# Performance work log

Hardware: AMD Instinct MI355X
Metric: run time of the kernel (lower is better)

The kernel has to match this reference:

```python
import jax, jax.numpy as jnp
import numpy as np

B = 65536
D_MODEL = 2048
N_EXPERTS = 64
TOP_K = 8
AUX_COEF = 0.01


def setup_inputs() -> dict:
    key = jax.random.key(0)
    kx, kw = jax.random.split(key)
    x = jax.random.normal(kx, (B, D_MODEL), dtype=jnp.float32)
    # nn.Linear(d_model, n_experts, bias=False); stored here as (d_model, n_experts)
    W = jax.random.normal(kw, (D_MODEL, N_EXPERTS), dtype=jnp.float32) / np.sqrt(D_MODEL).astype(np.float32)
    expert_bias = jnp.zeros((N_EXPERTS,), dtype=jnp.float32)
    return {"x": x, "W": W, "expert_bias": expert_bias}


def reference(x, W, expert_bias):
    # router logits: (B, n_experts)
    logits = x @ W
    # topk on bias-shifted logits (aux-loss-free balancing bias)
    biased = logits + expert_bias
    _, indices = jax.lax.top_k(biased, TOP_K)              # (B, top_k) int32
    # softmax over the UNbiased logits of the selected experts
    selected = jnp.take_along_axis(logits, indices, axis=-1)  # (B, top_k)
    gates_topk = jax.nn.softmax(selected, axis=-1)
    # scatter gate weights into sparse (B, n_experts) tensor
    rows = jnp.arange(logits.shape[0])[:, None]
    gates = jnp.zeros_like(logits).at[rows, indices].set(gates_topk)
    # aux load-balance loss (training mode): fraction routed * mean prob
    f_i = (gates > 0).astype(logits.dtype).mean(axis=0)       # (n_experts,)
    P_i = jax.nn.softmax(logits, axis=-1).mean(axis=0)        # (n_experts,)
    aux_loss = AUX_COEF * N_EXPERTS * jnp.sum(f_i * P_i)
    return gates, indices, aux_loss
```

## Files before the change

### kernel.cpp

```cpp
#include <hip/hip_runtime.h>
#include <cstdint>
#include <cstddef>

typedef __attribute__((ext_vector_type(8))) short short8;
typedef __attribute__((ext_vector_type(4))) float f32x4;

#define B_ROWS 65536
#define DMODEL 2048
#define NEXP 64
#define TOPK 8
#define THREADS 256
#define ROWS_PER_BLK 64
#define NBLK (B_ROWS / ROWS_PER_BLK)
#define NKS (DMODEL / 32)
#define SLAB 67
#define GOFF ((size_t)B_ROWS * NEXP)
#define AUX_OFF (GOFF + (size_t)B_ROWS * TOPK)
#define WS_FRAG_OFF 131072

#define GLOAD16(g, l)                                                      \
  __builtin_amdgcn_global_load_lds(                                       \
      (const __attribute__((address_space(1))) void*)(g),                 \
      (__attribute__((address_space(3))) void*)(l), 16, 0, 0)

__device__ __forceinline__ unsigned short bf16_rne(float v, float* back) {
  unsigned u = __float_as_uint(v);
  unsigned r = (u + 0x7FFFu + ((u >> 16) & 1u)) >> 16;
  *back = __uint_as_float(r << 16);
  return (unsigned short)r;
}

__global__ __launch_bounds__(256) void router_prep(
    const float* __restrict__ W, unsigned short* __restrict__ frag)
{
  const int ks = blockIdx.x;
  const int nt = threadIdx.x >> 6;
  const int lane = threadIdx.x & 63;
  const int krow = ks * 32 + (lane >> 4) * 8;
  const int col = nt * 16 + (lane & 15);
  short8 hv, mv, lv;
#pragma unroll
  for (int j = 0; j < 8; ++j) {
    float v = W[(size_t)(krow + j) * NEXP + col];
    float fh, fm, fl;
    unsigned short h = bf16_rne(v, &fh);
    float r = v - fh;
    unsigned short m = bf16_rne(r, &fm);
    float r2 = r - fm;
    unsigned short l = bf16_rne(r2, &fl);
    hv[j] = (short)h; mv[j] = (short)m; lv[j] = (short)l;
  }
  size_t base = (size_t)(ks * 4 + nt) * 1536 + lane * 8;
  *(short8*)(frag + base)        = hv;
  *(short8*)(frag + base + 512)  = mv;
  *(short8*)(frag + base + 1024) = lv;
}

__device__ __forceinline__ void cvt3(float4 a, float4 b,
                                     short8* H, short8* M, short8* L) {
  float f[8] = {a.x, a.y, a.z, a.w, b.x, b.y, b.z, b.w};
#pragma unroll
  for (int j = 0; j < 8; ++j) {
    float fh, fm, fl;
    unsigned short h = bf16_rne(f[j], &fh);
    float r = f[j] - fh;
    unsigned short m = bf16_rne(r, &fm);
    float r2 = r - fm;
    unsigned short l = bf16_rne(r2, &fl);
    (*H)[j] = (short)h; (*M)[j] = (short)m; (*L)[j] = (short)l;
  }
}

#define MFMA __builtin_amdgcn_mfma_f32_16x16x32_bf16

__global__ __launch_bounds__(THREADS, 4) void router_main(
    const float* __restrict__ x, const float* __restrict__ bias,
    const unsigned short* __restrict__ frag, float* __restrict__ out,
    float* __restrict__ ws)
{
  __shared__ __align__(16) float lds[6144];

  const int tid = threadIdx.x;
  const int lane = tid & 63;
  const int w = tid >> 6;
  const size_t row0 = (size_t)blockIdx.x * ROWS_PER_BLK;

  f32x4 acc[4];
#pragma unroll
  for (int nt = 0; nt < 4; ++nt) acc[nt] = (f32x4){0.f, 0.f, 0.f, 0.f};

  const float* xp = x + (row0 + (size_t)w * 16 + (lane & 15)) * DMODEL
                  + (lane >> 4) * 8;

#define STAGE(KS, BUF)                                                     \
  do {                                                                     \
    _Pragma("unroll") for (int j = 0; j < 3; ++j)                          \
      GLOAD16(frag + (size_t)(KS) * 6144 + (w * 3 + j) * 512 + lane * 8,   \
              lds + (BUF) * 3072 + (w * 3 + j) * 256);                     \
  } while (0)

  STAGE(0, 0);
  float4 c0 = *(const float4*)(xp);
  float4 c1 = *(const float4*)(xp + 4);

  for (int ks = 0; ks < NKS; ++ks) {
    __syncthreads();
    float4 n0, n1;
    if (ks + 1 < NKS) {
      STAGE(ks + 1, (ks + 1) & 1);
      n0 = *(const float4*)(xp + (ks + 1) * 32);
      n1 = *(const float4*)(xp + (ks + 1) * 32 + 4);
    }
    const float* bb = lds + (ks & 1) * 3072;
    short8 B[12];
#pragma unroll
    for (int f = 0; f < 12; ++f)
      B[f] = *(const short8*)(bb + f * 256 + lane * 4);
    short8 Ah, Am, Al;
    cvt3(c0, c1, &Ah, &Am, &Al);
#pragma unroll
    for (int nt = 0; nt < 4; ++nt) {
      acc[nt] = MFMA(Ah, B[nt * 3 + 0], acc[nt], 0, 0, 0);
      acc[nt] = MFMA(Ah, B[nt * 3 + 1], acc[nt], 0, 0, 0);
      acc[nt] = MFMA(Am, B[nt * 3 + 0], acc[nt], 0, 0, 0);
      acc[nt] = MFMA(Am, B[nt * 3 + 1], acc[nt], 0, 0, 0);
      acc[nt] = MFMA(Ah, B[nt * 3 + 2], acc[nt], 0, 0, 0);
      acc[nt] = MFMA(Al, B[nt * 3 + 0], acc[nt], 0, 0, 0);
    }
    if (ks + 1 < NKS) { c0 = n0; c1 = n1; }
  }

  __syncthreads();
  float* slab = lds;
#pragma unroll
  for (int nt = 0; nt < 4; ++nt)
#pragma unroll
    for (int reg = 0; reg < 4; ++reg) {
      int row = w * 16 + (lane >> 4) * 4 + reg;
      int col = nt * 16 + (lane & 15);
      slab[row * SLAB + col] = acc[nt][reg];
    }
  __syncthreads();

  if (w == 0) {
    float a[NEXP];
#pragma unroll
    for (int n = 0; n < NEXP; ++n) a[n] = slab[lane * SLAB + n];

    unsigned long long sel = 0ull;
    int idx[TOPK];
    float selu[TOPK];
#pragma unroll
    for (int k = 0; k < TOPK; ++k) {
      float best = -INFINITY, bestu = 0.f;
      int bi = 0;
#pragma unroll
      for (int n = 0; n < NEXP; ++n) {
        float vb = a[n] + bias[n];
        bool taken = (sel >> n) & 1ull;
        vb = taken ? -INFINITY : vb;
        if (vb > best) { best = vb; bestu = a[n]; bi = n; }
      }
      sel |= 1ull << bi;
      idx[k] = bi;
      selu[k] = bestu;
    }

    float mx = selu[0];
#pragma unroll
    for (int k = 1; k < TOPK; ++k) mx = fmaxf(mx, selu[k]);
    float g[TOPK]; float gs = 0.f;
#pragma unroll
    for (int k = 0; k < TOPK; ++k) { g[k] = __expf(selu[k] - mx); gs += g[k]; }
    float ginv = 1.f / gs;

    float* grow = out + (row0 + lane) * NEXP;
#pragma unroll
    for (int n4 = 0; n4 < 16; ++n4) {
      float gv[4];
#pragma unroll
      for (int j = 0; j < 4; ++j) {
        int n = n4 * 4 + j;
        float v = 0.f;
#pragma unroll
        for (int k = 0; k < TOPK; ++k) v = (idx[k] == n) ? g[k] * ginv : v;
        gv[j] = v;
      }
      *(float4*)(grow + n4 * 4) = make_float4(gv[0], gv[1], gv[2], gv[3]);
    }

    float* irow = out + GOFF + (row0 + lane) * TOPK;
    *(float4*)(irow + 0) = make_float4((float)idx[0], (float)idx[1], (float)idx[2], (float)idx[3]);
    *(float4*)(irow + 4) = make_float4((float)idx[4], (float)idx[5], (float)idx[6], (float)idx[7]);

    float m2 = -INFINITY;
#pragma unroll
    for (int n = 0; n < NEXP; ++n) m2 = fmaxf(m2, a[n]);
    float s2 = 0.f;
#pragma unroll
    for (int n = 0; n < NEXP; ++n) s2 += __expf(a[n] - m2);
    float pinv = 1.f / s2;

    float myP = 0.f, myF = 0.f;
#pragma unroll
    for (int n = 0; n < NEXP; ++n) {
      float v = __expf(a[n] - m2) * pinv;
      v += __shfl_xor(v, 1);
      v += __shfl_xor(v, 2);
      v += __shfl_xor(v, 4);
      v += __shfl_xor(v, 8);
      v += __shfl_xor(v, 16);
      v += __shfl_xor(v, 32);
      unsigned long long b = __ballot((sel >> n) & 1ull);
      if (lane == n) { myP = v; myF = (float)__popcll(b); }
    }
    ws[(size_t)blockIdx.x * (2 * NEXP) + lane] = myF;
    ws[(size_t)blockIdx.x * (2 * NEXP) + NEXP + lane] = myP;
  }
}

__global__ __launch_bounds__(256) void router_aux(
    const float* __restrict__ ws, float* __restrict__ out)
{
  __shared__ float sf[4][NEXP];
  __shared__ float sp[4][NEXP];
  int t = threadIdx.x;
  int n = t & 63, part = t >> 6;
  float f = 0.f, p = 0.f;
#pragma unroll 8
  for (int b = part; b < NBLK; b += 4) {
    f += ws[(size_t)b * (2 * NEXP) + n];
    p += ws[(size_t)b * (2 * NEXP) + NEXP + n];
  }
  sf[part][n] = f;
  sp[part][n] = p;
  __syncthreads();
  if (t < NEXP) {
    float F = sf[0][t] + sf[1][t] + sf[2][t] + sf[3][t];
    float P = sp[0][t] + sp[1][t] + sp[2][t] + sp[3][t];
    float v = F * P;
    v += __shfl_xor(v, 1);
    v += __shfl_xor(v, 2);
    v += __shfl_xor(v, 4);
    v += __shfl_xor(v, 8);
    v += __shfl_xor(v, 16);
    v += __shfl_xor(v, 32);
    if (t == 0)
      out[AUX_OFF] = 0.01f * 64.f * v / (4294967296.0f );
  }
}

extern "C" void kernel_launch(void* const* d_in, const int* in_sizes, int n_in,
                              void* d_out, int out_size, void* d_ws, size_t ws_size,
                              hipStream_t stream) {
  const float* x = (const float*)d_in[0];
  const float* W = (const float*)d_in[1];
  const float* bias = (const float*)d_in[2];
  float* out = (float*)d_out;
  float* ws = (float*)d_ws;
  unsigned short* frag = (unsigned short*)(ws + WS_FRAG_OFF);
  router_prep<<<NKS, 256, 0, stream>>>(W, frag);
  router_main<<<NBLK, THREADS, 0, stream>>>(x, bias, frag, out, ws);
  router_aux<<<1, 256, 0, stream>>>(ws, out);
}
```

Before: 216.2 us.

## Stage x tiles into LDS via async global_load_lds and split aux reduction

The main kernel now loads x in 128-column chunks (four k-steps) straight into LDS using async global-to-LDS loads instead of per-thread float4 register loads. The goal is fewer, larger memory transactions that overlap with the MFMA work. This raises LDS use, so occupancy hints drop from 4 to 2 blocks per CU, and there is a manual vmcnt wait. The single-block aux reduction is also split into a 16-block partial pass and a final 64-thread pass, which adds a kernel launch.

```diff
diff --git a/kernel.cpp b/kernel.cpp
--- a/kernel.cpp
+++ b/kernel.cpp
@@ -17,6 +17,10 @@
 #define GOFF ((size_t)B_ROWS * NEXP)
 #define AUX_OFF (GOFF + (size_t)B_ROWS * TOPK)
 #define WS_FRAG_OFF 131072
+#define WS2_OFF 229376
+#define XW 2080
+#define BBASE 8320
+#define LDSF 14464
 
 #define GLOAD16(g, l)                                                      \
   __builtin_amdgcn_global_load_lds(                                       \
@@ -73,12 +77,12 @@
 
 #define MFMA __builtin_amdgcn_mfma_f32_16x16x32_bf16
 
-__global__ __launch_bounds__(THREADS, 4) void router_main(
+__global__ __launch_bounds__(THREADS, 2) void router_main(
     const float* __restrict__ x, const float* __restrict__ bias,
     const unsigned short* __restrict__ frag, float* __restrict__ out,
     float* __restrict__ ws)
 {
-  __shared__ __align__(16) float lds[6144];
+  __shared__ __align__(16) float lds[LDSF];
 
   const int tid = threadIdx.x;
   const int lane = tid & 63;
@@ -89,33 +93,47 @@
 #pragma unroll
   for (int nt = 0; nt < 4; ++nt) acc[nt] = (f32x4){0.f, 0.f, 0.f, 0.f};
 
-  const float* xp = x + (row0 + (size_t)w * 16 + (lane & 15)) * DMODEL
-                  + (lane >> 4) * 8;
-
-#define STAGE(KS, BUF)                                                     \
+  const float* xg = x + (row0 + (size_t)w * 16 + (lane >> 5)) * DMODEL
+                  + (lane & 31) * 4;
+  const int xr_off = w * XW + ((lane & 15) >> 1) * 260 + ((lane & 15) & 1) * 128
+                   + (lane >> 4) * 8;
+
+#define STAGE_X(SC)                                                        \
+  do {                                                                     \
+    _Pragma("unroll") for (int i = 0; i < 8; ++i)                          \
+      GLOAD16(xg + (size_t)i * 2 * DMODEL + (SC) * 128,                    \
+              lds + w * XW + i * 260);                                     \
+  } while (0)
+
+#define STAGE_B(KS, BUF)                                                   \
   do {                                                                     \
     _Pragma("unroll") for (int j = 0; j < 3; ++j)                          \
       GLOAD16(frag + (size_t)(KS) * 6144 + (w * 3 + j) * 512 + lane * 8,   \
-              lds + (BUF) * 3072 + (w * 3 + j) * 256);                     \
+              lds + BBASE + (BUF) * 3072 + (w * 3 + j) * 256);             \
   } while (0)
 
-  STAGE(0, 0);
-  float4 c0 = *(const float4*)(xp);
-  float4 c1 = *(const float4*)(xp + 4);
+  STAGE_X(0);
+  STAGE_B(0, 0);
 
   for (int ks = 0; ks < NKS; ++ks) {
     __syncthreads();
-    float4 n0, n1;
-    if (ks + 1 < NKS) {
-      STAGE(ks + 1, (ks + 1) & 1);
-      n0 = *(const float4*)(xp + (ks + 1) * 32);
-      n1 = *(const float4*)(xp + (ks + 1) * 32 + 4);
-    }
-    const float* bb = lds + (ks & 1) * 3072;
+    if ((ks & 3) == 0 && ks > 0) {
+      STAGE_X(ks >> 2);
+      if (ks + 1 < NKS) STAGE_B(ks + 1, (ks + 1) & 1);
+      asm volatile("s_waitcnt vmcnt(3)" ::: "memory");
+      __builtin_amdgcn_sched_barrier(0);
+    } else {
+      if (ks + 1 < NKS) STAGE_B(ks + 1, (ks + 1) & 1);
+    }
+
+    const float* bb = lds + BBASE + (ks & 1) * 3072;
     short8 B[12];
 #pragma unroll
     for (int f = 0; f < 12; ++f)
       B[f] = *(const short8*)(bb + f * 256 + lane * 4);
+
+    float4 c0 = *(const float4*)(lds + xr_off + (ks & 3) * 32);
+    float4 c1 = *(const float4*)(lds + xr_off + (ks & 3) * 32 + 4);
     short8 Ah, Am, Al;
     cvt3(c0, c1, &Ah, &Am, &Al);
 #pragma unroll
@@ -127,7 +145,6 @@
       acc[nt] = MFMA(Ah, B[nt * 3 + 2], acc[nt], 0, 0, 0);
       acc[nt] = MFMA(Al, B[nt * 3 + 0], acc[nt], 0, 0, 0);
     }
-    if (ks + 1 < NKS) { c0 = n0; c1 = n1; }
   }
 
   __syncthreads();
@@ -219,16 +236,17 @@
   }
 }
 
-__global__ __launch_bounds__(256) void router_aux(
-    const float* __restrict__ ws, float* __restrict__ out)
+__global__ __launch_bounds__(256) void router_aux1(
+    const float* __restrict__ ws, float* __restrict__ ws2)
 {
   __shared__ float sf[4][NEXP];
   __shared__ float sp[4][NEXP];
   int t = threadIdx.x;
   int n = t & 63, part = t >> 6;
+  int b0 = blockIdx.x * 64;
   float f = 0.f, p = 0.f;
-#pragma unroll 8
-  for (int b = part; b < NBLK; b += 4) {
+#pragma unroll 4
+  for (int b = b0 + part; b < b0 + 64; b += 4) {
     f += ws[(size_t)b * (2 * NEXP) + n];
     p += ws[(size_t)b * (2 * NEXP) + NEXP + n];
   }
@@ -236,18 +254,30 @@
   sp[part][n] = p;
   __syncthreads();
   if (t < NEXP) {
-    float F = sf[0][t] + sf[1][t] + sf[2][t] + sf[3][t];
-    float P = sp[0][t] + sp[1][t] + sp[2][t] + sp[3][t];
-    float v = F * P;
-    v += __shfl_xor(v, 1);
-    v += __shfl_xor(v, 2);
-    v += __shfl_xor(v, 4);
-    v += __shfl_xor(v, 8);
-    v += __shfl_xor(v, 16);
-    v += __shfl_xor(v, 32);
-    if (t == 0)
-      out[AUX_OFF] = 0.01f * 64.f * v / (4294967296.0f );
-  }
+    ws2[blockIdx.x * 128 + t]      = sf[0][t] + sf[1][t] + sf[2][t] + sf[3][t];
+    ws2[blockIdx.x * 128 + 64 + t] = sp[0][t] + sp[1][t] + sp[2][t] + sp[3][t];
+  }
+}
+
+__global__ __launch_bounds__(64) void router_aux2(
+    const float* __restrict__ ws2, float* __restrict__ out)
+{
+  int t = threadIdx.x;
+  float F = 0.f, P = 0.f;
+#pragma unroll
+  for (int g = 0; g < 16; ++g) {
+    F += ws2[g * 128 + t];
+    P += ws2[g * 128 + 64 + t];
+  }
+  float v = F * P;
+  v += __shfl_xor(v, 1);
+  v += __shfl_xor(v, 2);
+  v += __shfl_xor(v, 4);
+  v += __shfl_xor(v, 8);
+  v += __shfl_xor(v, 16);
+  v += __shfl_xor(v, 32);
+  if (t == 0)
+    out[AUX_OFF] = 0.01f * 64.f * v / (4294967296.0f );
 }
 
 extern "C" void kernel_launch(void* const* d_in, const int* in_sizes, int n_in,
@@ -259,7 +289,9 @@
   float* out = (float*)d_out;
   float* ws = (float*)d_ws;
   unsigned short* frag = (unsigned short*)(ws + WS_FRAG_OFF);
+  float* ws2 = ws + WS2_OFF;
   router_prep<<<NKS, 256, 0, stream>>>(W, frag);
   router_main<<<NBLK, THREADS, 0, stream>>>(x, bias, frag, out, ws);
-  router_aux<<<1, 256, 0, stream>>>(ws, out);
-}
+  router_aux1<<<16, 256, 0, stream>>>(ws, ws2);
+  router_aux2<<<1, 64, 0, stream>>>(ws2, out);
+}
```

Result: slower. 232.8 us (+7.7%).
